# Kernel optimization log

Hardware: AMD Instinct MI355X
Metric: run time of the kernel (lower is better)

The kernel has to match this reference:

```python
import jax, jax.numpy as jnp
import numpy as np
from jax import lax

PERIODS = [1, 2, 4, 8]
N = 128  # output_dim // len(periods)
INPUT_DIM = 512
OUTPUT_DIM = 512
BATCH = 64
SEQ = 512


def setup_inputs() -> dict:
    key = jax.random.key(0)
    ks = jax.random.split(key, 32)
    inp = {}
    inp['x'] = jax.random.normal(ks[0], (BATCH, SEQ, INPUT_DIM), dtype=jnp.float32)
    s = 0.05
    inp['W'] = jax.random.normal(ks[1], (INPUT_DIM, OUTPUT_DIM), dtype=jnp.float32) * s
    inp['b'] = jnp.zeros((OUTPUT_DIM,), dtype=jnp.float32)
    inp['Wr'] = jax.random.normal(ks[2], (INPUT_DIM, OUTPUT_DIM), dtype=jnp.float32) * s
    inp['br'] = jnp.zeros((OUTPUT_DIM,), dtype=jnp.float32)
    inp['Wz'] = jax.random.normal(ks[3], (INPUT_DIM, OUTPUT_DIM), dtype=jnp.float32) * s
    inp['bz'] = jnp.zeros((OUTPUT_DIM,), dtype=jnp.float32)
    kidx = 4
    for i in range(len(PERIODS)):
        m = (i + 1) * N
        inp[f'clock_h_{i}'] = jax.random.normal(ks[kidx], (m, N), dtype=jnp.float32) * (1.0 / np.sqrt(m)); kidx += 1
        inp[f'clock_r_{i}'] = jax.random.normal(ks[kidx], (m, m), dtype=jnp.float32) * (1.0 / np.sqrt(m)); kidx += 1
        inp[f'clock_z_{i}'] = jax.random.normal(ks[kidx], (m, N), dtype=jnp.float32) * (1.0 / np.sqrt(m)); kidx += 1
    return inp


def _forward(x, W, b, Wr, br, Wz, bz, clock_h, clock_r, clock_z):
    # x: [B, S, D_in] -> time-major [S, B, D_in]
    Xt = jnp.transpose(x, (1, 0, 2))
    xt = Xt @ W + b      # [S, B, D]
    xrt = Xt @ Wr + br   # [S, B, D]
    xzt = Xt @ Wz + bz   # [S, B, D]
    B = x.shape[0]
    D = W.shape[1]

    def step(h, inputs):
        t, x_t, x_rt, x_zt = inputs
        blocks = []
        for i, period in enumerate(PERIODS):
            m = (i + 1) * N
            hp = h[:, :m]                 # [B, (i+1)n]
            nah = h[:, i * N:(i + 1) * N] # [B, n]
            r = jax.nn.sigmoid(x_rt[:, :m] + hp @ clock_r[i])
            z = jax.nn.sigmoid(x_zt[:, i * N:(i + 1) * N] + hp @ clock_z[i])
            h_new = jax.nn.sigmoid(x_t[:, i * N:(i + 1) * N] + (r * hp) @ clock_h[i])
            v = z * h_new + (1.0 - z) * nah
            blocks.append(jnp.where(t % period == 0, v, nah))
        h_t = jnp.concatenate(blocks, axis=1)
        return h_t, h_t

    times = jnp.arange(x.shape[1])
    h0 = jnp.zeros((B, D), dtype=x.dtype)
    _, hs = lax.scan(step, h0, (times, xt, xrt, xzt))
    # return_sequences=True: back to batch-major [B, S, D]
    return jnp.transpose(hs, (1, 0, 2))


def reference(x, W, b, Wr, br, Wz, bz,
              clock_h_0, clock_r_0, clock_z_0,
              clock_h_1, clock_r_1, clock_z_1,
              clock_h_2, clock_r_2, clock_z_2,
              clock_h_3, clock_r_3, clock_z_3):
    clock_h = [clock_h_0, clock_h_1, clock_h_2, clock_h_3]
    clock_r = [clock_r_0, clock_r_1, clock_r_2, clock_r_3]
    clock_z = [clock_z_0, clock_z_1, clock_z_2, clock_z_3]
    return _forward(x, W, b, Wr, br, Wz, bz, clock_h, clock_r, clock_z)
```

## Files before the change

### kernel.cpp

```cpp
#include <hip/hip_runtime.h>

#define SEQ   512
#define BATCH 64
#define DIM   512

typedef float  f32x4 __attribute__((ext_vector_type(4)));
typedef short  s16x8 __attribute__((ext_vector_type(8)));
typedef __bf16 bf16x2 __attribute__((ext_vector_type(2)));

__device__ __forceinline__ float bits2f(unsigned u) {
  union { unsigned u; float f; } v; v.u = u; return v.f;
}
__device__ __forceinline__ float bf2f(unsigned short h) { return bits2f((unsigned)h << 16); }
__device__ __forceinline__ float bflo(unsigned u) { return bits2f(u << 16); }
__device__ __forceinline__ float bfhi(unsigned u) { return bits2f(u & 0xFFFF0000u); }
__device__ __forceinline__ unsigned short f2bf(float f) {
  union { float f; unsigned u; } v; v.f = f;
  unsigned r = v.u + 0x7FFFu + ((v.u >> 16) & 1u);
  return (unsigned short)(r >> 16);
}
__device__ __forceinline__ unsigned packbf(float lo, float hi) {
  return (unsigned)f2bf(lo) | ((unsigned)f2bf(hi) << 16);
}
__device__ __forceinline__ float sigm(float x) { return 1.0f / (1.0f + __expf(-x)); }

__device__ __forceinline__ float dot2(unsigned w, unsigned h, float acc) {
#if __has_builtin(__builtin_amdgcn_fdot2_f32_bf16)
  return __builtin_amdgcn_fdot2_f32_bf16(__builtin_bit_cast(bf16x2, w),
                                         __builtin_bit_cast(bf16x2, h), acc, false);
#else
  return acc + bflo(w) * bflo(h) + bfhi(w) * bfhi(h);
#endif
}

__device__ __forceinline__ void bar_lds() {
  asm volatile("s_waitcnt lgkmcnt(0)" ::: "memory");
  __builtin_amdgcn_s_barrier();
  asm volatile("" ::: "memory");
}

#define NJOBS 18
struct CastJobs {
  const float* src[NJOBS];
  const float* src2[NJOBS];
  void*        dst[NJOBS];
  int          n[NJOBS];
  int          mode[NJOBS];
  int          m[NJOBS];
  int          iN[NJOBS];
};

__global__ __launch_bounds__(256) void cast_kernel(CastJobs jobs) {
  int gsz = gridDim.x * blockDim.x;
  int gid = blockIdx.x * blockDim.x + threadIdx.x;
  for (int j = 0; j < NJOBS; ++j) {
    int n = jobs.n[j], mode = jobs.mode[j];
    int m = jobs.m[j], iN = jobs.iN[j];
    const float* s = jobs.src[j];
    if (mode == 1) {
      unsigned short* d = (unsigned short*)jobs.dst[j];
      for (int i = gid; i < n; i += gsz) {
        int k = i >> 9, nn = i & 511;
        d[nn * 512 + k] = f2bf(s[i]);
      }
    } else if (mode == 3) {
      unsigned* d = (unsigned*)jobs.dst[j];
      for (int i = gid; i < n; i += gsz) {
        int k2 = i / m, jj = i - k2 * m;
        d[i] = packbf(s[(iN + 2 * k2) * m + jj], s[(iN + 2 * k2 + 1) * m + jj]);
      }
    } else if (mode == 4) {
      unsigned* d = (unsigned*)jobs.dst[j];
      for (int i = gid; i < n; i += gsz) {
        int k2 = i >> 7, jj = i & 127;
        d[i] = packbf(s[(2 * k2) * 128 + jj], s[(2 * k2 + 1) * 128 + jj]);
      }
    } else if (mode == 5) {
      unsigned* d = (unsigned*)jobs.dst[j];
      for (int i = gid; i < n; i += gsz) {
        int k2 = i >> 7, jj = i & 127;
        d[i] = packbf(s[(iN + 2 * k2) * 128 + jj], s[(iN + 2 * k2 + 1) * 128 + jj]);
      }
    } else if (mode == 6) {
      const float* s2 = jobs.src2[j];
      unsigned short* d = (unsigned short*)jobs.dst[j];
      for (int i = gid; i < n; i += gsz) {
        int nrow = i / iN, k = i - nrow * iN;
        float v = (nrow < m) ? s[k * m + nrow] : s2[k * 128 + (nrow - m)];
        d[i] = f2bf(v);
      }
    }
  }
}

__global__ __launch_bounds__(256) void proj_kernel(
    const float* __restrict__ x,
    const unsigned short* __restrict__ WbT,
    const float* __restrict__ bias0, const float* __restrict__ bias1,
    const float* __restrict__ bias2,
    unsigned short* __restrict__ p0, unsigned short* __restrict__ p1,
    unsigned short* __restrict__ p2)
{
  __shared__ __align__(16) unsigned short aS[64 * 40];
  __shared__ __align__(16) unsigned short bS[128 * 40];

  int bx = blockIdx.x;
  int nt = bx % 12, t = bx / 12;
  int wsel = nt >> 2, ncol0 = (nt & 3) * 128;
  const float* bias = (wsel == 0) ? bias0 : (wsel == 1 ? bias1 : bias2);
  unsigned short* pout = (wsel == 0) ? p0 : (wsel == 1 ? p1 : p2);

  int tid = threadIdx.x;
  int wv = tid >> 6, lane = tid & 63;
  int lq = lane & 15, quad = lane >> 4;

  f32x4 acc[8];
#pragma unroll
  for (int s = 0; s < 8; ++s) acc[s] = (f32x4){0.f, 0.f, 0.f, 0.f};

  int arow = tid >> 2, ak0 = (tid & 3) * 8;
  const float* asrc0 = x + ((size_t)arow * SEQ + t) * DIM + ak0;
  int brow = tid >> 1, bk0 = (tid & 1) * 16;
  const unsigned short* bsrc0 =
      WbT + ((size_t)(wsel * 512 + ncol0 + brow)) * 512 + bk0;

  for (int kk = 0; kk < 16; ++kk) {
    const float* asrc = asrc0 + kk * 32;
    float4 f0 = *(const float4*)(asrc);
    float4 f1 = *(const float4*)(asrc + 4);
    uint4 av;
    av.x = packbf(f0.x, f0.y);
    av.y = packbf(f0.z, f0.w);
    av.z = packbf(f1.x, f1.y);
    av.w = packbf(f1.z, f1.w);
    *(uint4*)(aS + arow * 40 + ak0) = av;
    const unsigned short* bsrc = bsrc0 + kk * 32;
    *(uint4*)(bS + brow * 40 + bk0)     = *(const uint4*)(bsrc);
    *(uint4*)(bS + brow * 40 + bk0 + 8) = *(const uint4*)(bsrc + 8);
    __syncthreads();

    s16x8 af = *(const s16x8*)(aS + (wv * 16 + lq) * 40 + quad * 8);
#pragma unroll
    for (int s = 0; s < 8; ++s) {
      s16x8 bf = *(const s16x8*)(bS + (s * 16 + lq) * 40 + quad * 8);
      acc[s] = __builtin_amdgcn_mfma_f32_16x16x32_bf16(af, bf, acc[s], 0, 0, 0);
    }
    __syncthreads();
  }

#pragma unroll
  for (int s = 0; s < 8; ++s) {
    int col = ncol0 + s * 16 + lq;
    float bv = bias[col];
#pragma unroll
    for (int v = 0; v < 4; ++v) {
      int b = wv * 16 + quad * 4 + v;
      pout[((size_t)(t * BATCH + b)) * DIM + col] = f2bf(acc[s][v] + bv);
    }
  }
}

template<int I>
__global__ __launch_bounds__(256) void base_gemm(
    const float* __restrict__ outp,
    const unsigned short* __restrict__ Bcat,
    unsigned short* __restrict__ baseO)
{
  constexpr int KI  = 4 * I;
  constexpr int K   = 128 * I;
  constexpr int NT  = I + 2;
  constexpr int NW  = NT * 128;
  constexpr int PER = 1 << I;

  __shared__ __align__(16) unsigned short aS[64 * 40];
  __shared__ __align__(16) unsigned short bS[128 * 40];

  int bx = blockIdx.x;
  int nt = bx % NT, n = bx / NT;
  int ncol0 = nt * 128;

  int tid = threadIdx.x;
  int wv = tid >> 6, lane = tid & 63;
  int lq = lane & 15, quad = lane >> 4;

  f32x4 acc[8];
#pragma unroll
  for (int s = 0; s < 8; ++s) acc[s] = (f32x4){0.f, 0.f, 0.f, 0.f};

  int arow = tid >> 2, ak0 = (tid & 3) * 8;
  const float* asrc0 = outp + ((size_t)arow * SEQ + (n * PER - 1)) * DIM + ak0;
  int brow = tid >> 1, bk0 = (tid & 1) * 16;
  const unsigned short* bsrc0 = Bcat + (size_t)(ncol0 + brow) * K + bk0;

  for (int kk = 0; kk < KI; ++kk) {
    uint4 av;
    if (n > 0) {
      const float* asrc = asrc0 + kk * 32;
      float4 f0 = *(const float4*)(asrc);
      float4 f1 = *(const float4*)(asrc + 4);
      av.x = packbf(f0.x, f0.y);
      av.y = packbf(f0.z, f0.w);
      av.z = packbf(f1.x, f1.y);
      av.w = packbf(f1.z, f1.w);
    } else {
      av = (uint4){0u, 0u, 0u, 0u};
    }
    *(uint4*)(aS + arow * 40 + ak0) = av;
    const unsigned short* bsrc = bsrc0 + kk * 32;
    *(uint4*)(bS + brow * 40 + bk0)     = *(const uint4*)(bsrc);
    *(uint4*)(bS + brow * 40 + bk0 + 8) = *(const uint4*)(bsrc + 8);
    __syncthreads();

    s16x8 af = *(const s16x8*)(aS + (wv * 16 + lq) * 40 + quad * 8);
#pragma unroll
    for (int s = 0; s < 8; ++s) {
      s16x8 bf = *(const s16x8*)(bS + (s * 16 + lq) * 40 + quad * 8);
      acc[s] = __builtin_amdgcn_mfma_f32_16x16x32_bf16(af, bf, acc[s], 0, 0, 0);
    }
    __syncthreads();
  }

#pragma unroll
  for (int s = 0; s < 8; ++s) {
    int col = ncol0 + s * 16 + lq;
#pragma unroll
    for (int v = 0; v < 4; ++v) {
      int bb = wv * 16 + quad * 4 + v;
      baseO[(size_t)(n * 64 + bb) * NW + col] = f2bf(acc[s][v]);
    }
  }
}

template<int I, int TPB>
__global__ __launch_bounds__(TPB, 1) void scan_phase(
    const unsigned short* __restrict__ px,
    const unsigned short* __restrict__ pr,
    const unsigned short* __restrict__ pz,
    const unsigned* __restrict__ crpk,
    const unsigned* __restrict__ czpk,
    const unsigned* __restrict__ chpk,
    const unsigned short* __restrict__ base,
    float* __restrict__ out)
{
  constexpr int M   = (I + 1) * 128;
  constexpr int IN  = I * 128;
  constexpr int PER = 1 << I;
  constexpr int U   = 512 >> I;
  constexpr int NW  = M + 128;
  constexpr int HKP = M / 2;
  constexpr int SPL = (I == 0) ? 2 : 4;
  constexpr int HT  = HKP / SPL;
  constexpr int ZT  = 64 / SPL;
  constexpr int RTH = (M < TPB) ? M : TPB;

  __shared__ __align__(16) float    hS[128];
  __shared__ __align__(16) unsigned hPk[64];
  __shared__ __align__(16) unsigned uPk[HKP];

  const int b  = blockIdx.x;
  const int t  = threadIdx.x;
  const int jh = t / SPL;
  const int q  = t % SPL;
  const bool hasR = (t < RTH);
  const int col0 = t;

  unsigned wr0[64];
  if (hasR) {
#pragma unroll
    for (int k2 = 0; k2 < 64; ++k2) wr0[k2] = crpk[k2 * M + col0];
  }
  unsigned wz[ZT];
#pragma unroll
  for (int k2 = 0; k2 < ZT; ++k2) wz[k2] = czpk[(q * ZT + k2) * 128 + jh];
  unsigned wh[HT];
#pragma unroll
  for (int k2 = 0; k2 < HT; ++k2) wh[k2] = chpk[(q * HT + k2) * 128 + jh];

  if (t < 128) hS[t] = 0.f;
  if (t < 64)  hPk[t] = 0u;
  float vprev = 0.f;

  unsigned short f_pr = 0, f_pz = 0, f_px = 0, f_br = 0, f_bz = 0;
  float f_pv = 0.f;
  {
    f_pz = (pz + (size_t)b * DIM)[IN + jh];
    f_px = (px + (size_t)b * DIM)[IN + jh];
    if (hasR) f_pr = (pr + (size_t)b * DIM)[col0];
    if constexpr (I > 0) {
      const unsigned short* baseR = base + (size_t)b * NW;
      if (hasR) f_br = baseR[col0];
      f_bz = baseR[M + jh];
    }
  }

  bar_lds();

  for (int n = 0; n < U; ++n) {
    const int s = n * PER;
    const unsigned short c_pr = f_pr, c_pz = f_pz, c_px = f_px;
    const unsigned short c_br = f_br, c_bz = f_bz;
    const float c_pv = f_pv;

    {
      const int n2 = (n + 1 < U) ? (n + 1) : n;
      const int s2 = n2 * PER;
      f_pz = (pz + ((size_t)(s2 * BATCH + b)) * DIM)[IN + jh];
      f_px = (px + ((size_t)(s2 * BATCH + b)) * DIM)[IN + jh];
      if (hasR) f_pr = (pr + ((size_t)(s2 * BATCH + b)) * DIM)[col0];
      if constexpr (I > 0) {
        const unsigned short* baseR = base + (size_t)(n2 * 64 + b) * NW;
        if (hasR) f_br = baseR[col0];
        f_bz = baseR[M + jh];
        if (hasR && col0 < IN)
          f_pv = (out + ((size_t)b * SEQ + (s2 - 1)) * DIM)[col0];
      }
    }

    float az0 = 0.f, az1 = 0.f;
#pragma unroll
    for (int k2 = 0; k2 < ZT; k2 += 2) {
      az0 = dot2(wz[k2],     hPk[q * ZT + k2],     az0);
      az1 = dot2(wz[k2 + 1], hPk[q * ZT + k2 + 1], az1);
    }
    float az = az0 + az1;
    az += __shfl_xor(az, 1);
    if constexpr (SPL == 4) az += __shfl_xor(az, 2);
    float zpre = bf2f(c_pz) + az;
    if constexpr (I > 0) zpre += bf2f(c_bz);
    const float zg = sigm(zpre);

    float u = 0.f;
    if (hasR) {
      float a0 = 0.f, a1 = 0.f, a2 = 0.f, a3 = 0.f;
#pragma unroll
      for (int k2 = 0; k2 < 64; k2 += 4) {
        a0 = dot2(wr0[k2],     hPk[k2],     a0);
        a1 = dot2(wr0[k2 + 1], hPk[k2 + 1], a1);
        a2 = dot2(wr0[k2 + 2], hPk[k2 + 2], a2);
        a3 = dot2(wr0[k2 + 3], hPk[k2 + 3], a3);
      }
      float ar = bf2f(c_pr) + (a0 + a1) + (a2 + a3);
      if constexpr (I > 0) ar += bf2f(c_br);
      const float r = sigm(ar);
      float hp;
      if constexpr (I == 0) hp = hS[col0];
      else hp = (col0 >= IN) ? hS[col0 - IN] : c_pv;
      u = r * hp;
    }
    const float uo = __shfl_xor(u, 1);
    if (hasR && !(t & 1)) uPk[t >> 1] = packbf(u, uo);

    bar_lds();

    float ah0 = 0.f, ah1 = 0.f, ah2 = 0.f, ah3 = 0.f;
    {
      const int o = q * HT;
#pragma unroll
      for (int k2 = 0; k2 < HT; k2 += 4) {
        ah0 = dot2(wh[k2],     uPk[o + k2],     ah0);
        ah1 = dot2(wh[k2 + 1], uPk[o + k2 + 1], ah1);
        ah2 = dot2(wh[k2 + 2], uPk[o + k2 + 2], ah2);
        ah3 = dot2(wh[k2 + 3], uPk[o + k2 + 3], ah3);
      }
    }
    float ah = (ah0 + ah1) + (ah2 + ah3);
    ah += __shfl_xor(ah, 1);
    if constexpr (SPL == 4) ah += __shfl_xor(ah, 2);
    const float hnew = sigm(ah + bf2f(c_px));
    const float v = zg * hnew + (1.f - zg) * vprev;
    vprev = v;

    if (q == 0) hS[jh] = v;
    const float vp = __shfl_xor(v, SPL);
    if ((t & (2 * SPL - 1)) == 0) hPk[t / (2 * SPL)] = packbf(v, vp);

    float* orow = out + ((size_t)b * SEQ + s) * DIM + IN + jh;
#pragma unroll
    for (int p = q; p < PER; p += SPL) orow[p * DIM] = v;

    bar_lds();
  }
}

extern "C" void kernel_launch(void* const* d_in, const int* in_sizes, int n_in,
                              void* d_out, int out_size, void* d_ws, size_t ws_size,
                              hipStream_t stream) {
  (void)in_sizes; (void)n_in; (void)out_size; (void)ws_size;

  const float* x  = (const float*)d_in[0];
  const float* W  = (const float*)d_in[1];
  const float* bb = (const float*)d_in[2];
  const float* Wr = (const float*)d_in[3];
  const float* br = (const float*)d_in[4];
  const float* Wz = (const float*)d_in[5];
  const float* bz = (const float*)d_in[6];
  const float* ch_[4]; const float* cr_[4]; const float* cz_[4];
  for (int i = 0; i < 4; ++i) {
    ch_[i] = (const float*)d_in[7 + 3 * i];
    cr_[i] = (const float*)d_in[8 + 3 * i];
    cz_[i] = (const float*)d_in[9 + 3 * i];
  }

  char* ws = (char*)d_ws;
  size_t off = 0;
  auto alloc = [&](size_t bytes) -> void* {
    void* p = ws + off;
    off += (bytes + 255) & ~(size_t)255;
    return p;
  };

  unsigned short* WbT = (unsigned short*)alloc(3ull * 512 * 512 * 2);
  unsigned* Crpk[4]; unsigned* Chpk[4]; unsigned* Czpk[4];
  unsigned short* Bcat[4] = {nullptr, nullptr, nullptr, nullptr};
  for (int i = 0; i < 4; ++i) {
    int m = (i + 1) * 128;
    Crpk[i] = (unsigned*)alloc((size_t)64 * m * 4);
    Chpk[i] = (unsigned*)alloc((size_t)(m / 2) * 128 * 4);
    Czpk[i] = (unsigned*)alloc((size_t)64 * 128 * 4);
  }
  for (int i = 1; i < 4; ++i) {
    int m = (i + 1) * 128, iN = i * 128;
    Bcat[i] = (unsigned short*)alloc((size_t)(m + 128) * iN * 2);
  }
  unsigned short* p0 = (unsigned short*)alloc((size_t)SEQ * BATCH * DIM * 2);
  unsigned short* p1 = (unsigned short*)alloc((size_t)SEQ * BATCH * DIM * 2);
  unsigned short* p2 = (unsigned short*)alloc((size_t)SEQ * BATCH * DIM * 2);
  unsigned short* baseB = (unsigned short*)alloc((size_t)16384 * 384 * 2);

  CastJobs jobs{};
  int jn = 0;
  const float* wsrc[3] = {W, Wr, Wz};
  for (int j = 0; j < 3; ++j) {
    jobs.src[jn] = wsrc[j]; jobs.dst[jn] = WbT + (size_t)j * 512 * 512;
    jobs.n[jn] = 512 * 512; jobs.mode[jn] = 1; jobs.m[jn] = 512; jobs.iN[jn] = 0; jn++;
  }
  for (int i = 0; i < 4; ++i) {
    int m = (i + 1) * 128, iN = i * 128;
    jobs.src[jn] = cr_[i]; jobs.dst[jn] = Crpk[i];
    jobs.n[jn] = 64 * m; jobs.mode[jn] = 3; jobs.m[jn] = m; jobs.iN[jn] = iN; jn++;
    jobs.src[jn] = ch_[i]; jobs.dst[jn] = Chpk[i];
    jobs.n[jn] = (m / 2) * 128; jobs.mode[jn] = 4; jobs.m[jn] = m; jobs.iN[jn] = iN; jn++;
    jobs.src[jn] = cz_[i]; jobs.dst[jn] = Czpk[i];
    jobs.n[jn] = 64 * 128; jobs.mode[jn] = 5; jobs.m[jn] = m; jobs.iN[jn] = iN; jn++;
  }
  for (int i = 1; i < 4; ++i) {
    int m = (i + 1) * 128, iN = i * 128;
    jobs.src[jn] = cr_[i]; jobs.src2[jn] = cz_[i]; jobs.dst[jn] = Bcat[i];
    jobs.n[jn] = (m + 128) * iN; jobs.mode[jn] = 6; jobs.m[jn] = m; jobs.iN[jn] = iN; jn++;
  }
  cast_kernel<<<256, 256, 0, stream>>>(jobs);

  proj_kernel<<<SEQ * 12, 256, 0, stream>>>(x, WbT, bb, br, bz, p0, p1, p2);

  float* outp = (float*)d_out;

  scan_phase<0, 256><<<64, 256, 0, stream>>>(p0, p1, p2, Crpk[0], Czpk[0],
                                             Chpk[0], nullptr, outp);
  base_gemm<1><<<256 * 3, 256, 0, stream>>>(outp, Bcat[1], baseB);
  scan_phase<1, 512><<<64, 512, 0, stream>>>(p0, p1, p2, Crpk[1], Czpk[1],
                                             Chpk[1], baseB, outp);
  base_gemm<2><<<128 * 4, 256, 0, stream>>>(outp, Bcat[2], baseB);
  scan_phase<2, 512><<<64, 512, 0, stream>>>(p0, p1, p2, Crpk[2], Czpk[2],
                                             Chpk[2], baseB, outp);
  base_gemm<3><<<64 * 5, 256, 0, stream>>>(outp, Bcat[3], baseB);
  scan_phase<3, 512><<<64, 512, 0, stream>>>(p0, p1, p2, Crpk[3], Czpk[3],
                                             Chpk[3], baseB, outp);
}
```

Before: 1.514 ms.

## Replace phase-0 scan with single-wave kernel holding weights in registers

Phase 0 of the recurrence (the period-1 block) moves from a 256-thread block to one 64-lane wave per batch row, with each lane owning two output columns. All three recurrent weight matrices stay in registers, and block barriers are replaced by LDS waitcnt fences, which is enough because only one wave runs per block. Gate inputs are prefetched two steps ahead to hide global latency. The cost is heavy register pressure (384 weight registers per lane, so spills are possible) and far fewer active threads per step.

```diff
diff --git a/kernel.cpp b/kernel.cpp
--- a/kernel.cpp
+++ b/kernel.cpp
@@ -37,6 +37,10 @@
   asm volatile("s_waitcnt lgkmcnt(0)" ::: "memory");
   __builtin_amdgcn_s_barrier();
   asm volatile("" ::: "memory");
+}
+
+__device__ __forceinline__ void fence_lds() {
+  asm volatile("s_waitcnt lgkmcnt(0)" ::: "memory");
 }
 
 #define NJOBS 18
@@ -228,6 +232,102 @@
       int bb = wv * 16 + quad * 4 + v;
       baseO[(size_t)(n * 64 + bb) * NW + col] = f2bf(acc[s][v]);
     }
+  }
+}
+
+__global__ __launch_bounds__(64, 1) void scan0_wave(
+    const unsigned short* __restrict__ px,
+    const unsigned short* __restrict__ pr,
+    const unsigned short* __restrict__ pz,
+    const unsigned* __restrict__ crpk,
+    const unsigned* __restrict__ czpk,
+    const unsigned* __restrict__ chpk,
+    float* __restrict__ out)
+{
+  __shared__ __align__(16) unsigned hPkS[64];
+  __shared__ __align__(16) unsigned uPkS[64];
+
+  const int b = blockIdx.x;
+  const int l = threadIdx.x;
+  const int c0 = 2 * l;
+
+  unsigned wr0[64], wr1[64], wz0[64], wz1[64], wh0[64], wh1[64];
+#pragma unroll
+  for (int k2 = 0; k2 < 64; ++k2) {
+    uint2 r2 = *(const uint2*)(crpk + k2 * 128 + c0);
+    uint2 z2 = *(const uint2*)(czpk + k2 * 128 + c0);
+    uint2 h2 = *(const uint2*)(chpk + k2 * 128 + c0);
+    wr0[k2] = r2.x; wr1[k2] = r2.y;
+    wz0[k2] = z2.x; wz1[k2] = z2.y;
+    wh0[k2] = h2.x; wh1[k2] = h2.y;
+  }
+
+  hPkS[l] = 0u;
+  float v0 = 0.f, v1 = 0.f;
+
+  size_t r0o = ((size_t)(0 * BATCH + b)) * DIM + c0;
+  size_t r1o = ((size_t)(1 * BATCH + b)) * DIM + c0;
+  unsigned f_pr = *(const unsigned*)(pr + r0o);
+  unsigned f_pz = *(const unsigned*)(pz + r0o);
+  unsigned f_px = *(const unsigned*)(px + r0o);
+  unsigned g_pr = *(const unsigned*)(pr + r1o);
+  unsigned g_pz = *(const unsigned*)(pz + r1o);
+  unsigned g_px = *(const unsigned*)(px + r1o);
+
+  fence_lds();
+
+  for (int s = 0; s < SEQ; ++s) {
+    const unsigned c_pr = f_pr, c_pz = f_pz, c_px = f_px;
+    f_pr = g_pr; f_pz = g_pz; f_px = g_px;
+    {
+      const int s2 = (s + 2 < SEQ) ? (s + 2) : (SEQ - 1);
+      const size_t ro = ((size_t)(s2 * BATCH + b)) * DIM + c0;
+      g_pr = *(const unsigned*)(pr + ro);
+      g_pz = *(const unsigned*)(pz + ro);
+      g_px = *(const unsigned*)(px + ro);
+    }
+
+    float ar0 = 0.f, ar0b = 0.f, ar1 = 0.f, ar1b = 0.f;
+    float az0 = 0.f, az0b = 0.f, az1 = 0.f, az1b = 0.f;
+#pragma unroll
+    for (int k2 = 0; k2 < 64; k2 += 2) {
+      unsigned h0 = hPkS[k2], h1 = hPkS[k2 + 1];
+      ar0  = dot2(wr0[k2],     h0, ar0);
+      ar0b = dot2(wr0[k2 + 1], h1, ar0b);
+      ar1  = dot2(wr1[k2],     h0, ar1);
+      ar1b = dot2(wr1[k2 + 1], h1, ar1b);
+      az0  = dot2(wz0[k2],     h0, az0);
+      az0b = dot2(wz0[k2 + 1], h1, az0b);
+      az1  = dot2(wz1[k2],     h0, az1);
+      az1b = dot2(wz1[k2 + 1], h1, az1b);
+    }
+    const float r0 = sigm(bflo(c_pr) + ar0 + ar0b);
+    const float r1 = sigm(bfhi(c_pr) + ar1 + ar1b);
+    const float z0 = sigm(bflo(c_pz) + az0 + az0b);
+    const float z1 = sigm(bfhi(c_pz) + az1 + az1b);
+
+    uPkS[l] = packbf(r0 * v0, r1 * v1);
+    fence_lds();
+
+    float ah0 = 0.f, ah0b = 0.f, ah1 = 0.f, ah1b = 0.f;
+#pragma unroll
+    for (int k2 = 0; k2 < 64; k2 += 2) {
+      unsigned u0 = uPkS[k2], u1 = uPkS[k2 + 1];
+      ah0  = dot2(wh0[k2],     u0, ah0);
+      ah0b = dot2(wh0[k2 + 1], u1, ah0b);
+      ah1  = dot2(wh1[k2],     u0, ah1);
+      ah1b = dot2(wh1[k2 + 1], u1, ah1b);
+    }
+    const float hn0 = sigm(bflo(c_px) + ah0 + ah0b);
+    const float hn1 = sigm(bfhi(c_px) + ah1 + ah1b);
+    v0 = z0 * hn0 + (1.f - z0) * v0;
+    v1 = z1 * hn1 + (1.f - z1) * v1;
+
+    hPkS[l] = packbf(v0, v1);
+    fence_lds();
+
+    float2 vv; vv.x = v0; vv.y = v1;
+    *(float2*)(out + ((size_t)b * SEQ + s) * DIM + c0) = vv;
   }
 }
 
@@ -454,8 +554,7 @@
 
   float* outp = (float*)d_out;
 
-  scan_phase<0, 256><<<64, 256, 0, stream>>>(p0, p1, p2, Crpk[0], Czpk[0],
-                                             Chpk[0], nullptr, outp);
+  scan0_wave<<<64, 64, 0, stream>>>(p0, p1, p2, Crpk[0], Czpk[0], Chpk[0], outp);
   base_gemm<1><<<256 * 3, 256, 0, stream>>>(outp, Bcat[1], baseB);
   scan_phase<1, 512><<<64, 512, 0, stream>>>(p0, p1, p2, Crpk[1], Czpk[1],
                                              Chpk[1], baseB, outp);
```

New measurement: 2.026 ms. 33.8% more time.

## Restructure recurrent scan with readlane broadcasts and warp-specialized r/z threads

Applied to the files above, without the earlier changes.

Replaces the scan kernel with a version in which threads below M compute the reset gate and a split-K slice of the candidate matmul, while an extra group of 128 threads computes the update gate in parallel. The hidden state and the reset-scaled vector are broadcast through v_readlane from a register rather than read from LDS for every dot product, and candidate partial sums are reduced through a small LDS buffer. Block sizes change per phase (256/384/512/640 threads), and weights are pinned in registers with asm barriers. This is meant to cut LDS traffic and serial dependence per timestep, at the cost of one more barrier per step, more registers, and many scalar readlane instructions.

```diff
diff --git a/kernel.cpp b/kernel.cpp
--- a/kernel.cpp
+++ b/kernel.cpp
@@ -31,6 +31,10 @@
 #else
   return acc + bflo(w) * bflo(h) + bfhi(w) * bfhi(h);
 #endif
+}
+
+__device__ __forceinline__ unsigned bcast(unsigned v, int k2) {
+  return (unsigned)__builtin_amdgcn_readlane((int)v, k2);
 }
 
 __device__ __forceinline__ void bar_lds() {
@@ -231,154 +235,179 @@
   }
 }
 
-template<int I, int TPB>
-__global__ __launch_bounds__(TPB, 1) void scan_phase(
-    const unsigned short* __restrict__ px,
-    const unsigned short* __restrict__ pr,
-    const unsigned short* __restrict__ pz,
-    const unsigned* __restrict__ crpk,
-    const unsigned* __restrict__ czpk,
-    const unsigned* __restrict__ chpk,
-    const unsigned short* __restrict__ base,
-    float* __restrict__ out)
+template<int I>
+__global__ __launch_bounds__((I + 2) * 128, (I == 3) ? 3 : ((I >= 1) ? 2 : 1))
+void scan_rl(const unsigned short* __restrict__ px,
+             const unsigned short* __restrict__ pr,
+             const unsigned short* __restrict__ pz,
+             const unsigned* __restrict__ crpk,
+             const unsigned* __restrict__ czpk,
+             const unsigned* __restrict__ chpk,
+             const unsigned short* __restrict__ base,
+             float* __restrict__ out)
 {
-  constexpr int M   = (I + 1) * 128;
-  constexpr int IN  = I * 128;
-  constexpr int PER = 1 << I;
-  constexpr int U   = 512 >> I;
-  constexpr int NW  = M + 128;
-  constexpr int HKP = M / 2;
-  constexpr int SPL = (I == 0) ? 2 : 4;
-  constexpr int HT  = HKP / SPL;
-  constexpr int ZT  = 64 / SPL;
-  constexpr int RTH = (M < TPB) ? M : TPB;
-
-  __shared__ __align__(16) float    hS[128];
-  __shared__ __align__(16) unsigned hPk[64];
-  __shared__ __align__(16) unsigned uPk[HKP];
-
-  const int b  = blockIdx.x;
-  const int t  = threadIdx.x;
-  const int jh = t / SPL;
-  const int q  = t % SPL;
-  const bool hasR = (t < RTH);
-  const int col0 = t;
-
-  unsigned wr0[64];
-  if (hasR) {
-#pragma unroll
-    for (int k2 = 0; k2 < 64; ++k2) wr0[k2] = crpk[k2 * M + col0];
-  }
-  unsigned wz[ZT];
-#pragma unroll
-  for (int k2 = 0; k2 < ZT; ++k2) wz[k2] = czpk[(q * ZT + k2) * 128 + jh];
-  unsigned wh[HT];
-#pragma unroll
-  for (int k2 = 0; k2 < HT; ++k2) wh[k2] = chpk[(q * HT + k2) * 128 + jh];
-
-  if (t < 128) hS[t] = 0.f;
-  if (t < 64)  hPk[t] = 0u;
+  constexpr int M    = (I + 1) * 128;
+  constexpr int IN   = I * 128;
+  constexpr int PER  = 1 << I;
+  constexpr int U    = 512 >> I;
+  constexpr int NW   = M + 128;
+  constexpr int SPL2 = I + 1;
+
+  __shared__ float    hF[128];
+  __shared__ unsigned hX[64];
+  __shared__ unsigned uX[M / 2];
+  __shared__ float    zX[128];
+  __shared__ float    partX[(SPL2 > 1) ? (SPL2 - 1) * 128 : 1];
+
+  const int  b   = blockIdx.x;
+  const int  t   = threadIdx.x;
+  const bool isR = (t < M);
+  const int  jz  = t - M;
+  const int  q   = t >> 7;
+  const bool isF = (t < 128);
+
+  unsigned wr[64], wh[64], wz[64];
+  if (isR) {
+#pragma unroll
+    for (int k2 = 0; k2 < 64; ++k2) wr[k2] = crpk[k2 * M + t];
+#pragma unroll
+    for (int k2 = 0; k2 < 64; ++k2) asm volatile("" : "+v"(wr[k2]));
+#pragma unroll
+    for (int k2 = 0; k2 < 64; ++k2) wh[k2] = chpk[(q * 64 + k2) * 128 + (t & 127)];
+#pragma unroll
+    for (int k2 = 0; k2 < 64; ++k2) asm volatile("" : "+v"(wh[k2]));
+  } else {
+#pragma unroll
+    for (int k2 = 0; k2 < 64; ++k2) wz[k2] = czpk[k2 * 128 + jz];
+#pragma unroll
+    for (int k2 = 0; k2 < 64; ++k2) asm volatile("" : "+v"(wz[k2]));
+  }
+
+  if (isF) hF[t] = 0.f;
+  unsigned hpk = 0u;
   float vprev = 0.f;
 
-  unsigned short f_pr = 0, f_pz = 0, f_px = 0, f_br = 0, f_bz = 0;
+  constexpr size_t STRD = (size_t)PER * BATCH * DIM;
+  unsigned short f_pr = 0, f_br = 0, f_pz = 0, f_bz = 0, f_px = 0;
   float f_pv = 0.f;
-  {
-    f_pz = (pz + (size_t)b * DIM)[IN + jh];
-    f_px = (px + (size_t)b * DIM)[IN + jh];
-    if (hasR) f_pr = (pr + (size_t)b * DIM)[col0];
+  const unsigned short* prp = nullptr;
+  const unsigned short* pxp = nullptr;
+  const unsigned short* pzp = nullptr;
+  const unsigned short* bsp = nullptr;
+  const float* pvp = nullptr;
+  if (isR) {
+    f_pr = pr[(size_t)b * DIM + t];
+    prp  = pr + ((size_t)PER * BATCH + b) * DIM + t;
     if constexpr (I > 0) {
-      const unsigned short* baseR = base + (size_t)b * NW;
-      if (hasR) f_br = baseR[col0];
-      f_bz = baseR[M + jh];
-    }
-  }
+      f_br = base[(size_t)b * NW + t];
+      bsp  = base + ((size_t)64 + b) * NW + t;
+      if (t < IN) pvp = out + ((size_t)b * SEQ + (PER - 1)) * DIM + t;
+    }
+    if (isF) {
+      f_px = px[(size_t)b * DIM + IN + t];
+      pxp  = px + ((size_t)PER * BATCH + b) * DIM + IN + t;
+    }
+  } else {
+    f_pz = pz[(size_t)b * DIM + IN + jz];
+    pzp  = pz + ((size_t)PER * BATCH + b) * DIM + IN + jz;
+    if constexpr (I > 0) {
+      f_bz = base[(size_t)b * NW + M + jz];
+      bsp  = base + ((size_t)64 + b) * NW + M + jz;
+    }
+  }
+  float* op = out + (size_t)b * SEQ * DIM + IN + (isF ? t : 0);
 
   bar_lds();
 
   for (int n = 0; n < U; ++n) {
-    const int s = n * PER;
-    const unsigned short c_pr = f_pr, c_pz = f_pz, c_px = f_px;
-    const unsigned short c_br = f_br, c_bz = f_bz;
+    const unsigned short c_pr = f_pr, c_br = f_br, c_pz = f_pz, c_bz = f_bz,
+                         c_px = f_px;
     const float c_pv = f_pv;
 
-    {
-      const int n2 = (n + 1 < U) ? (n + 1) : n;
-      const int s2 = n2 * PER;
-      f_pz = (pz + ((size_t)(s2 * BATCH + b)) * DIM)[IN + jh];
-      f_px = (px + ((size_t)(s2 * BATCH + b)) * DIM)[IN + jh];
-      if (hasR) f_pr = (pr + ((size_t)(s2 * BATCH + b)) * DIM)[col0];
-      if constexpr (I > 0) {
-        const unsigned short* baseR = base + (size_t)(n2 * 64 + b) * NW;
-        if (hasR) f_br = baseR[col0];
-        f_bz = baseR[M + jh];
-        if (hasR && col0 < IN)
-          f_pv = (out + ((size_t)b * SEQ + (s2 - 1)) * DIM)[col0];
-      }
-    }
-
-    float az0 = 0.f, az1 = 0.f;
-#pragma unroll
-    for (int k2 = 0; k2 < ZT; k2 += 2) {
-      az0 = dot2(wz[k2],     hPk[q * ZT + k2],     az0);
-      az1 = dot2(wz[k2 + 1], hPk[q * ZT + k2 + 1], az1);
-    }
-    float az = az0 + az1;
-    az += __shfl_xor(az, 1);
-    if constexpr (SPL == 4) az += __shfl_xor(az, 2);
-    float zpre = bf2f(c_pz) + az;
-    if constexpr (I > 0) zpre += bf2f(c_bz);
-    const float zg = sigm(zpre);
-
-    float u = 0.f;
-    if (hasR) {
+    if (n + 1 < U) {
+      if (isR) {
+        f_pr = *prp; prp += STRD;
+        if constexpr (I > 0) {
+          f_br = *bsp; bsp += (size_t)64 * NW;
+          if (t < IN) { f_pv = *pvp; pvp += (size_t)PER * DIM; }
+        }
+        if (isF) { f_px = *pxp; pxp += STRD; }
+      } else {
+        f_pz = *pzp; pzp += STRD;
+        if constexpr (I > 0) { f_bz = *bsp; bsp += (size_t)64 * NW; }
+      }
+    }
+
+    if (isR) {
       float a0 = 0.f, a1 = 0.f, a2 = 0.f, a3 = 0.f;
 #pragma unroll
       for (int k2 = 0; k2 < 64; k2 += 4) {
-        a0 = dot2(wr0[k2],     hPk[k2],     a0);
-        a1 = dot2(wr0[k2 + 1], hPk[k2 + 1], a1);
-        a2 = dot2(wr0[k2 + 2], hPk[k2 + 2], a2);
-        a3 = dot2(wr0[k2 + 3], hPk[k2 + 3], a3);
+        a0 = dot2(wr[k2],     bcast(hpk, k2),     a0);
+        a1 = dot2(wr[k2 + 1], bcast(hpk, k2 + 1), a1);
+        a2 = dot2(wr[k2 + 2], bcast(hpk, k2 + 2), a2);
+        a3 = dot2(wr[k2 + 3], bcast(hpk, k2 + 3), a3);
       }
       float ar = bf2f(c_pr) + (a0 + a1) + (a2 + a3);
       if constexpr (I > 0) ar += bf2f(c_br);
       const float r = sigm(ar);
       float hp;
-      if constexpr (I == 0) hp = hS[col0];
-      else hp = (col0 >= IN) ? hS[col0 - IN] : c_pv;
-      u = r * hp;
-    }
-    const float uo = __shfl_xor(u, 1);
-    if (hasR && !(t & 1)) uPk[t >> 1] = packbf(u, uo);
-
+      if constexpr (I == 0) hp = hF[t];
+      else hp = (t >= IN) ? hF[t - IN] : c_pv;
+      const float u  = r * hp;
+      const float uo = __shfl_xor(u, 1);
+      if (!(t & 1)) uX[t >> 1] = packbf(u, uo);
+    } else {
+      float a0 = 0.f, a1 = 0.f, a2 = 0.f, a3 = 0.f;
+#pragma unroll
+      for (int k2 = 0; k2 < 64; k2 += 4) {
+        a0 = dot2(wz[k2],     bcast(hpk, k2),     a0);
+        a1 = dot2(wz[k2 + 1], bcast(hpk, k2 + 1), a1);
+        a2 = dot2(wz[k2 + 2], bcast(hpk, k2 + 2), a2);
+        a3 = dot2(wz[k2 + 3], bcast(hpk, k2 + 3), a3);
+      }
+      float zp = bf2f(c_pz) + (a0 + a1) + (a2 + a3);
+      if constexpr (I > 0) zp += bf2f(c_bz);
+      zX[jz] = sigm(zp);
+    }
     bar_lds();
 
-    float ah0 = 0.f, ah1 = 0.f, ah2 = 0.f, ah3 = 0.f;
-    {
-      const int o = q * HT;
-#pragma unroll
-      for (int k2 = 0; k2 < HT; k2 += 4) {
-        ah0 = dot2(wh[k2],     uPk[o + k2],     ah0);
-        ah1 = dot2(wh[k2 + 1], uPk[o + k2 + 1], ah1);
-        ah2 = dot2(wh[k2 + 2], uPk[o + k2 + 2], ah2);
-        ah3 = dot2(wh[k2 + 3], uPk[o + k2 + 3], ah3);
-      }
-    }
-    float ah = (ah0 + ah1) + (ah2 + ah3);
-    ah += __shfl_xor(ah, 1);
-    if constexpr (SPL == 4) ah += __shfl_xor(ah, 2);
-    const float hnew = sigm(ah + bf2f(c_px));
-    const float v = zg * hnew + (1.f - zg) * vprev;
-    vprev = v;
-
-    if (q == 0) hS[jh] = v;
-    const float vp = __shfl_xor(v, SPL);
-    if ((t & (2 * SPL - 1)) == 0) hPk[t / (2 * SPL)] = packbf(v, vp);
-
-    float* orow = out + ((size_t)b * SEQ + s) * DIM + IN + jh;
-#pragma unroll
-    for (int p = q; p < PER; p += SPL) orow[p * DIM] = v;
-
+    float ah = 0.f;
+    if (isR) {
+      const unsigned upk = uX[(q << 6) | (t & 63)];
+      float a0 = 0.f, a1 = 0.f, a2 = 0.f, a3 = 0.f;
+#pragma unroll
+      for (int k2 = 0; k2 < 64; k2 += 4) {
+        a0 = dot2(wh[k2],     bcast(upk, k2),     a0);
+        a1 = dot2(wh[k2 + 1], bcast(upk, k2 + 1), a1);
+        a2 = dot2(wh[k2 + 2], bcast(upk, k2 + 2), a2);
+        a3 = dot2(wh[k2 + 3], bcast(upk, k2 + 3), a3);
+      }
+      ah = (a0 + a1) + (a2 + a3);
+      if constexpr (SPL2 > 1) {
+        if (q > 0) partX[(q - 1) * 128 + (t & 127)] = ah;
+      }
+    }
+    if constexpr (SPL2 > 1) bar_lds();
+
+    if (isF) {
+      float tot = ah;
+      if constexpr (SPL2 > 1) {
+#pragma unroll
+        for (int j = 1; j < SPL2; ++j) tot += partX[(j - 1) * 128 + t];
+      }
+      const float hnew = sigm(tot + bf2f(c_px));
+      const float z    = zX[t];
+      const float v    = z * hnew + (1.f - z) * vprev;
+      vprev = v;
+      hF[t] = v;
+      const float vo = __shfl_xor(v, 1);
+      if (!(t & 1)) hX[t >> 1] = packbf(v, vo);
+#pragma unroll
+      for (int p = 0; p < PER; ++p) op[p * DIM] = v;
+    }
+    op += (size_t)PER * DIM;
     bar_lds();
+    hpk = hX[t & 63];
   }
 }
 
@@ -454,15 +483,15 @@
 
   float* outp = (float*)d_out;
 
-  scan_phase<0, 256><<<64, 256, 0, stream>>>(p0, p1, p2, Crpk[0], Czpk[0],
-                                             Chpk[0], nullptr, outp);
+  scan_rl<0><<<64, 256, 0, stream>>>(p0, p1, p2, Crpk[0], Czpk[0], Chpk[0],
+                                     nullptr, outp);
   base_gemm<1><<<256 * 3, 256, 0, stream>>>(outp, Bcat[1], baseB);
-  scan_phase<1, 512><<<64, 512, 0, stream>>>(p0, p1, p2, Crpk[1], Czpk[1],
-                                             Chpk[1], baseB, outp);
+  scan_rl<1><<<64, 384, 0, stream>>>(p0, p1, p2, Crpk[1], Czpk[1], Chpk[1],
+                                     baseB, outp);
   base_gemm<2><<<128 * 4, 256, 0, stream>>>(outp, Bcat[2], baseB);
-  scan_phase<2, 512><<<64, 512, 0, stream>>>(p0, p1, p2, Crpk[2], Czpk[2],
-                                             Chpk[2], baseB, outp);
+  scan_rl<2><<<64, 512, 0, stream>>>(p0, p1, p2, Crpk[2], Czpk[2], Chpk[2],
+                                     baseB, outp);
   base_gemm<3><<<64 * 5, 256, 0, stream>>>(outp, Bcat[3], baseB);
-  scan_phase<3, 512><<<64, 512, 0, stream>>>(p0, p1, p2, Crpk[3], Czpk[3],
-                                             Chpk[3], baseB, outp);
-}
+  scan_rl<3><<<64, 640, 0, stream>>>(p0, p1, p2, Crpk[3], Czpk[3], Chpk[3],
+                                     baseB, outp);
+}
```

Result: slower. 2.238 ms (+47.8%).

## Add readlane-broadcast scan kernel with dedicated r/z/h thread roles for phases 0-2

Applied to the files above, without the earlier changes.

Adds a new recurrent scan kernel that gives separate thread groups the r, z and h matvecs and keeps 64 packed bf16 weights per thread in registers. Hidden-state operands are broadcast with readlane instead of per-lane LDS reads. Phases 0-2 use it with larger blocks of 384, 640 and 896 threads. The aim is to cut per-step LDS traffic and raise parallelism inside the serial time loop, at the cost of extra barriers, higher register pressure and launch-bound changes. Phase 3 still uses the old kernel, which also gains a guard that zeroes c_pv on the first step.

```diff
diff --git a/kernel.cpp b/kernel.cpp
--- a/kernel.cpp
+++ b/kernel.cpp
@@ -31,6 +31,10 @@
 #else
   return acc + bflo(w) * bflo(h) + bfhi(w) * bfhi(h);
 #endif
+}
+
+__device__ __forceinline__ unsigned bcast(unsigned v, int k2) {
+  return (unsigned)__builtin_amdgcn_readlane((int)v, k2);
 }
 
 __device__ __forceinline__ void bar_lds() {
@@ -228,6 +232,172 @@
       int bb = wv * 16 + quad * 4 + v;
       baseO[(size_t)(n * 64 + bb) * NW + col] = f2bf(acc[s][v]);
     }
+  }
+}
+
+template<int I>
+__global__ __launch_bounds__(128 * (2 * I + 3), (I == 0) ? 2 : (I == 1 ? 3 : 4))
+void scan_rl2(const unsigned short* __restrict__ px,
+              const unsigned short* __restrict__ pr,
+              const unsigned short* __restrict__ pz,
+              const unsigned* __restrict__ crpk,
+              const unsigned* __restrict__ czpk,
+              const unsigned* __restrict__ chpk,
+              const unsigned short* __restrict__ base,
+              float* __restrict__ out)
+{
+  constexpr int M   = (I + 1) * 128;
+  constexpr int IN  = I * 128;
+  constexpr int PER = 1 << I;
+  constexpr int U   = 512 >> I;
+  constexpr int NW  = M + 128;
+  constexpr int NSL = I + 1;
+
+  __shared__ float    hF[128];
+  __shared__ unsigned hX[64];
+  __shared__ unsigned uX[M / 2];
+  __shared__ float    zX[128];
+  __shared__ float    partX[(NSL > 1) ? (NSL - 1) * 128 : 1];
+
+  const int  b    = blockIdx.x;
+  const int  t    = threadIdx.x;
+  const bool isRZ = (t < M + 128);
+  const bool isR  = (t < M);
+  const int  jz   = t - M;
+  const int  hidx = t - (M + 128);
+  const int  q    = hidx >> 7;
+  const int  jj   = hidx & 127;
+  const bool isF  = (!isRZ) && (q == 0);
+
+  const unsigned* wsrc;
+  int wS, wO;
+  if (isR)       { wsrc = crpk; wS = M;   wO = t; }
+  else if (isRZ) { wsrc = czpk; wS = 128; wO = jz; }
+  else           { wsrc = chpk; wS = 128; wO = q * 8192 + jj; }
+  unsigned w[64];
+#pragma unroll
+  for (int k2 = 0; k2 < 64; ++k2) w[k2] = wsrc[(size_t)k2 * wS + wO];
+
+  if (t < 128) hF[t] = 0.f;
+  if (t < 64)  hX[t] = 0u;
+  float vprev = 0.f;
+
+  constexpr size_t STRD = (size_t)PER * BATCH * DIM;
+  unsigned short f_p = 0, f_b = 0;
+  float f_pv = 0.f;
+  const unsigned short* pp = nullptr;
+  const unsigned short* bp = nullptr;
+  const float* vp = nullptr;
+  if (isR) {
+    f_p = pr[(size_t)b * DIM + t];
+    pp  = pr + ((size_t)PER * BATCH + b) * DIM + t;
+    if constexpr (I > 0) {
+      f_b = base[(size_t)b * NW + t];
+      bp  = base + ((size_t)64 + b) * NW + t;
+      if (t < IN) {
+        f_pv = 0.f;
+        vp   = out + ((size_t)b * SEQ + (PER - 1)) * DIM + t;
+      }
+    }
+  } else if (isRZ) {
+    f_p = pz[(size_t)b * DIM + IN + jz];
+    pp  = pz + ((size_t)PER * BATCH + b) * DIM + IN + jz;
+    if constexpr (I > 0) {
+      f_b = base[(size_t)b * NW + M + jz];
+      bp  = base + ((size_t)64 + b) * NW + M + jz;
+    }
+  } else if (isF) {
+    f_p = px[(size_t)b * DIM + IN + jj];
+    pp  = px + ((size_t)PER * BATCH + b) * DIM + IN + jj;
+  }
+  float* op = out + (size_t)b * SEQ * DIM + IN + (isF ? jj : 0);
+
+  bar_lds();
+
+#pragma unroll 1
+  for (int n = 0; n < U; ++n) {
+    const unsigned short c_p = f_p, c_b = f_b;
+    const float c_pv = f_pv;
+
+    unsigned hpk = 0u;
+    if (isRZ) hpk = hX[t & 63];
+
+    if (n + 1 < U) {
+      if (isR) {
+        f_p = *pp; pp += STRD;
+        if constexpr (I > 0) {
+          f_b = *bp; bp += (size_t)64 * NW;
+          if (t < IN) { f_pv = *vp; vp += (size_t)PER * DIM; }
+        }
+      } else if (isRZ) {
+        f_p = *pp; pp += STRD;
+        if constexpr (I > 0) { f_b = *bp; bp += (size_t)64 * NW; }
+      } else if (isF) {
+        f_p = *pp; pp += STRD;
+      }
+    }
+
+    if (isRZ) {
+      float a0 = 0.f, a1 = 0.f, a2 = 0.f, a3 = 0.f;
+#pragma unroll
+      for (int k2 = 0; k2 < 64; k2 += 4) {
+        a0 = dot2(w[k2],     bcast(hpk, k2),     a0);
+        a1 = dot2(w[k2 + 1], bcast(hpk, k2 + 1), a1);
+        a2 = dot2(w[k2 + 2], bcast(hpk, k2 + 2), a2);
+        a3 = dot2(w[k2 + 3], bcast(hpk, k2 + 3), a3);
+      }
+      float a = bf2f(c_p) + (a0 + a1) + (a2 + a3);
+      if constexpr (I > 0) a += bf2f(c_b);
+      if (isR) {
+        const float r = sigm(a);
+        float hp;
+        if constexpr (I == 0) hp = hF[t];
+        else hp = (t >= IN) ? hF[t - IN] : c_pv;
+        const float u  = r * hp;
+        const float uo = __shfl_xor(u, 1);
+        if (!(t & 1)) uX[t >> 1] = packbf(u, uo);
+      } else {
+        zX[jz] = sigm(a);
+      }
+    }
+    bar_lds();
+
+    float ah = 0.f, zf = 0.f;
+    if (!isRZ) {
+      const unsigned upk = uX[(q << 6) | (t & 63)];
+      if (isF) zf = zX[jj];
+      float a0 = 0.f, a1 = 0.f, a2 = 0.f, a3 = 0.f;
+#pragma unroll
+      for (int k2 = 0; k2 < 64; k2 += 4) {
+        a0 = dot2(w[k2],     bcast(upk, k2),     a0);
+        a1 = dot2(w[k2 + 1], bcast(upk, k2 + 1), a1);
+        a2 = dot2(w[k2 + 2], bcast(upk, k2 + 2), a2);
+        a3 = dot2(w[k2 + 3], bcast(upk, k2 + 3), a3);
+      }
+      ah = (a0 + a1) + (a2 + a3);
+      if constexpr (NSL > 1) {
+        if (q > 0) partX[(q - 1) * 128 + jj] = ah;
+      }
+    }
+    if constexpr (NSL > 1) bar_lds();
+
+    if (isF) {
+      float tot = ah;
+      if constexpr (NSL > 1) {
+#pragma unroll
+        for (int i = 1; i < NSL; ++i) tot += partX[(i - 1) * 128 + jj];
+      }
+      const float hnew = sigm(tot + bf2f(c_p));
+      const float v    = zf * hnew + (1.f - zf) * vprev;
+      vprev = v;
+      hF[jj] = v;
+      const float vo = __shfl_xor(v, 1);
+      if (!(jj & 1)) hX[jj >> 1] = packbf(v, vo);
+#pragma unroll
+      for (int p = 0; p < PER; ++p) op[p * DIM] = v;
+    }
+    op += (size_t)PER * DIM;
+    bar_lds();
   }
 }
 
@@ -253,9 +423,9 @@
   constexpr int ZT  = 64 / SPL;
   constexpr int RTH = (M < TPB) ? M : TPB;
 
-  __shared__ __align__(16) float    hS[128];
-  __shared__ __align__(16) unsigned hPk[64];
-  __shared__ __align__(16) unsigned uPk[HKP];
+  __shared__ float    hS[128];
+  __shared__ unsigned hPk[64];
+  __shared__ unsigned uPk[HKP];
 
   const int b  = blockIdx.x;
   const int t  = threadIdx.x;
@@ -344,7 +514,7 @@
       const float r = sigm(ar);
       float hp;
       if constexpr (I == 0) hp = hS[col0];
-      else hp = (col0 >= IN) ? hS[col0 - IN] : c_pv;
+      else hp = (col0 >= IN) ? hS[col0 - IN] : (n > 0 ? c_pv : 0.f);
       u = r * hp;
     }
     const float uo = __shfl_xor(u, 1);
@@ -454,14 +624,14 @@
 
   float* outp = (float*)d_out;
 
-  scan_phase<0, 256><<<64, 256, 0, stream>>>(p0, p1, p2, Crpk[0], Czpk[0],
-                                             Chpk[0], nullptr, outp);
+  scan_rl2<0><<<64, 384, 0, stream>>>(p0, p1, p2, Crpk[0], Czpk[0], Chpk[0],
+                                      nullptr, outp);
   base_gemm<1><<<256 * 3, 256, 0, stream>>>(outp, Bcat[1], baseB);
-  scan_phase<1, 512><<<64, 512, 0, stream>>>(p0, p1, p2, Crpk[1], Czpk[1],
-                                             Chpk[1], baseB, outp);
+  scan_rl2<1><<<64, 640, 0, stream>>>(p0, p1, p2, Crpk[1], Czpk[1], Chpk[1],
+                                      baseB, outp);
   base_gemm<2><<<128 * 4, 256, 0, stream>>>(outp, Bcat[2], baseB);
-  scan_phase<2, 512><<<64, 512, 0, stream>>>(p0, p1, p2, Crpk[2], Czpk[2],
-                                             Chpk[2], baseB, outp);
+  scan_rl2<2><<<64, 896, 0, stream>>>(p0, p1, p2, Crpk[2], Czpk[2], Chpk[2],
+                                      baseB, outp);
   base_gemm<3><<<64 * 5, 256, 0, stream>>>(outp, Bcat[3], baseB);
   scan_phase<3, 512><<<64, 512, 0, stream>>>(p0, p1, p2, Crpk[3], Czpk[3],
                                              Chpk[3], baseB, outp);
```

After: 1.970 ms. +30.1%, slower.
